# Performance work log

Hardware: AMD Instinct MI355X
Metric: run time of the kernel (lower is better)

## Reference

```python
import jax, jax.numpy as jnp
import numpy as np

DIM = 1024
HEADS = 16
HEAD_DIM = DIM // HEADS
K = 13              # kernel_size (odd)
NS = K // 2         # neighborhood radius
SCALE = HEAD_DIM ** -0.5


def setup_inputs() -> dict:
    key = jax.random.key(0)
    ks = jax.random.split(key, 5)
    B, L = 2, 4096
    x = jax.random.normal(ks[0], (B, L, DIM), jnp.float32)
    qkv_w = jax.random.normal(ks[1], (3 * DIM, DIM), jnp.float32) * 0.02
    qkv_b = jnp.zeros((3 * DIM,), jnp.float32)
    rpb = jax.random.normal(ks[2], (HEADS, 2 * K - 1), jnp.float32) * 0.02  # trunc_normal std=0.02
    proj_w = jax.random.normal(ks[3], (DIM, DIM), jnp.float32) * 0.02
    proj_b = jnp.zeros((DIM,), jnp.float32)
    return dict(x=x, qkv_w=qkv_w, qkv_b=qkv_b, rpb=rpb, proj_w=proj_w, proj_b=proj_b)


def reference(x, qkv_w, qkv_b, rpb, proj_w, proj_b):
    B, L, C = x.shape
    # qkv projection (torch Linear convention: y = x @ W^T + b)
    qkv = (x @ qkv_w.T + qkv_b).reshape(B, L, 3, HEADS, HEAD_DIM).transpose(2, 0, 3, 1, 4)
    q, k, v = qkv[0] * SCALE, qkv[1], qkv[2]  # each [B, H, L, D]

    i = jnp.arange(L)
    # NATTEN 1D window start (dilation=1): clamp window fully inside [0, L)
    ni = jnp.clip(i - NS, 0, L - K)                       # [L]
    # relative-position-bias start index per query (NATTEN get_pb_start)
    pi = NS + jnp.where(i < NS, NS - i, 0) + jnp.where(i + NS >= L, L - i - 1 - NS, 0)  # [L]
    j = jnp.arange(K)
    nbr = ni[:, None] + j[None, :]                        # [L, K] neighbor key indices
    bidx = pi[:, None] + j[None, :]                       # [L, K] rpb indices in [0, 2K-2]

    kg = k[:, :, nbr, :]                                  # [B, H, L, K, D]
    vg = v[:, :, nbr, :]                                  # [B, H, L, K, D]

    attn = jnp.einsum('bhld,bhlkd->bhlk', q, kg) + rpb[:, bidx][None]  # [B, H, L, K]
    attn = jax.nn.softmax(attn, axis=-1)
    out = jnp.einsum('bhlk,bhlkd->bhld', attn, vg)        # [B, H, L, D]
    out = out.transpose(0, 2, 1, 3).reshape(B, L, C)
    return out @ proj_w.T + proj_b
```

## Files before the change

### kernel.cpp

```cpp
#include <hip/hip_runtime.h>
#include <hip/hip_bf16.h>

#define DIMC 1024
#define HEADS 16
#define HEAD_DIM 64
#define KWIN 13
#define NSH 6
#define LSEQ 4096
#define BATCH 2
#define NROWS (BATCH*LSEQ)
#define QKV_N (3*DIMC)
#define SCALE_Q 0.125f

#define TBLK 256
#define WROWS 268

typedef __attribute__((ext_vector_type(4))) float f32x4;
typedef __attribute__((ext_vector_type(8))) short bf16x8;

__device__ __forceinline__ void gload_lds16(const void* g, void* l) {
  __builtin_amdgcn_global_load_lds(
      (const __attribute__((address_space(1))) void*)g,
      (__attribute__((address_space(3))) void*)l, 16, 0, 0);
}

__device__ __forceinline__ void cvt8(uint4 r, float* f) {
  unsigned u[4] = {r.x, r.y, r.z, r.w};
#pragma unroll
  for (int w = 0; w < 4; w++) {
    f[2*w]   = __uint_as_float(u[w] << 16);
    f[2*w+1] = __uint_as_float(u[w] & 0xffff0000u);
  }
}

__global__ __launch_bounds__(256) void cast3_kernel(const float* __restrict__ in0, __hip_bfloat16* __restrict__ out0, int n0,
                                                    const float* __restrict__ in1, __hip_bfloat16* __restrict__ out1, int n1,
                                                    const float* __restrict__ in2, __hip_bfloat16* __restrict__ out2, int n2) {
  int i = blockIdx.x * 256 + threadIdx.x;
  const float* in; __hip_bfloat16* out; int k;
  if (i < n0) { in = in0; out = out0; k = i; }
  else if (i < n0 + n1) { in = in1; out = out1; k = i - n0; }
  else if (i < n0 + n1 + n2) { in = in2; out = out2; k = i - n0 - n1; }
  else return;
  float4 v = ((const float4*)in)[k];
  union { short4 s; __hip_bfloat16 h[4]; } u;
  u.h[0] = __float2bfloat16(v.x);
  u.h[1] = __float2bfloat16(v.y);
  u.h[2] = __float2bfloat16(v.z);
  u.h[3] = __float2bfloat16(v.w);
  ((short4*)out)[k] = u.s;
}

template<int OUT_BF16>
__global__ __launch_bounds__(256) void gemm_bt(const __hip_bfloat16* __restrict__ A,
                                               const __hip_bfloat16* __restrict__ B,
                                               const float* __restrict__ bias,
                                               void* __restrict__ Cout,
                                               int M, int N, int K) {
  __shared__ __align__(16) __hip_bfloat16 smem[16384];
  __hip_bfloat16* As = smem;
  __hip_bfloat16* Bs = smem + 4096;

  const int tid  = threadIdx.x;
  const int lane = tid & 63;
  const int wave = tid >> 6;
  const int m0 = blockIdx.y * 128;
  const int n0 = blockIdx.x * 128;
  const int wr = wave >> 1;
  const int wc = wave & 1;

  f32x4 acc[4][4] = {};

  const int rA0  = wave * 32 + (lane >> 2);
  const int kcol = ((lane & 3) ^ ((lane >> 3) & 3)) * 8;
  const __hip_bfloat16* gA = A + (size_t)(m0 + rA0) * K + kcol;
  const __hip_bfloat16* gB = B + (size_t)(n0 + rA0) * K + kcol;
  __hip_bfloat16* lA0 = As + wave * 1024;
  __hip_bfloat16* lA1 = As + wave * 1024 + 512;
  __hip_bfloat16* lB0 = Bs + wave * 1024;
  __hip_bfloat16* lB1 = Bs + wave * 1024 + 512;

  const int fr  = lane & 15;
  const int fq  = lane >> 4;
  const int fk0 = ((fq ^ ((fr >> 1) & 3)) & 3) * 8;

  const size_t r16 = (size_t)16 * K;

  for (int k0 = 0; k0 < K; k0 += 64) {
    gload_lds16(gA,            lA0);
    gload_lds16(gA + r16,      lA1);
    gload_lds16(gB,            lB0);
    gload_lds16(gB + r16,      lB1);
    gload_lds16(gA + 32,       lA0 + 8192);
    gload_lds16(gA + r16 + 32, lA1 + 8192);
    gload_lds16(gB + 32,       lB0 + 8192);
    gload_lds16(gB + r16 + 32, lB1 + 8192);
    gA += 64;
    gB += 64;
    __syncthreads();

#pragma unroll
    for (int half = 0; half < 2; half++) {
      const int hb = half * 8192;
      bf16x8 af[4], bfr[4];
#pragma unroll
      for (int i = 0; i < 4; i++)
        af[i] = *(const bf16x8*)&As[hb + (wr * 64 + i * 16 + fr) * 32 + fk0];
#pragma unroll
      for (int i = 0; i < 4; i++)
        bfr[i] = *(const bf16x8*)&Bs[hb + (wc * 64 + i * 16 + fr) * 32 + fk0];

#pragma unroll
      for (int mi = 0; mi < 4; mi++)
#pragma unroll
        for (int ni = 0; ni < 4; ni++)
          acc[mi][ni] = __builtin_amdgcn_mfma_f32_16x16x32_bf16(af[mi], bfr[ni], acc[mi][ni], 0, 0, 0);
    }

    __syncthreads();
  }

#pragma unroll
  for (int ni = 0; ni < 4; ni++) {
    const int col = n0 + wc * 64 + ni * 16 + (lane & 15);
    const float bv = bias[col];
#pragma unroll
    for (int mi = 0; mi < 4; mi++) {
      const int row = m0 + wr * 64 + mi * 16 + ((lane >> 4) << 2);
#pragma unroll
      for (int i = 0; i < 4; i++) {
        const float v = acc[mi][ni][i] + bv;
        if (OUT_BF16)
          ((__hip_bfloat16*)Cout)[(size_t)(row + i) * N + col] = __float2bfloat16(v);
        else
          ((float*)Cout)[(size_t)(row + i) * N + col] = v;
      }
    }
  }
}

__global__ __launch_bounds__(256, 2) void natten(const __hip_bfloat16* __restrict__ qkv,
                                                 const float* __restrict__ rpb,
                                                 __hip_bfloat16* __restrict__ att) {
  __shared__ __align__(16) unsigned char smem[2 * WROWS * 128];

  const int tid = threadIdx.x;
  const int tb  = blockIdx.x;
  const int h   = blockIdx.y;
  const int b   = blockIdx.z;
  const int t0  = tb * TBLK;

  int r0 = t0 - NSH;
  if (r0 < 0) r0 = 0;
  if (r0 > LSEQ - WROWS) r0 = LSEQ - WROWS;

  const __hip_bfloat16* kg = qkv + ((size_t)b * LSEQ + r0) * QKV_N + DIMC + h * HEAD_DIM;
  const __hip_bfloat16* vg = kg + DIMC;
#pragma unroll 1
  for (int i = tid; i < WROWS * 8; i += 256) {
    const int row = i >> 3, c = i & 7;
    const uint4 kk = *(const uint4*)(kg + (size_t)row * QKV_N + c * 8);
    const uint4 vv = *(const uint4*)(vg + (size_t)row * QKV_N + c * 8);
    const int off = row * 128 + ((c * 16) ^ ((row & 7) << 4));
    *(uint4*)(smem + off) = kk;
    *(uint4*)(smem + WROWS * 128 + off) = vv;
  }
  __syncthreads();

  const int t = t0 + tid;
  int ni = t - NSH;
  ni = ni < 0 ? 0 : (ni > LSEQ - KWIN ? LSEQ - KWIN : ni);
  const int rbase = ni - r0;
  const int pi = NSH + (t < NSH ? NSH - t : 0) + (t + NSH >= LSEQ ? LSEQ - t - 1 - NSH : 0);
  const float* rp = rpb + h * (2 * KWIN - 1) + pi;

  const __hip_bfloat16* qg = qkv + ((size_t)b * LSEQ + t) * QKV_N + h * HEAD_DIM;
  float qf[64];
#pragma unroll
  for (int c = 0; c < 8; c++) {
    uint4 qq = *(const uint4*)(qg + c * 8);
    cvt8(qq, qf + c * 8);
  }

  float p[KWIN];
#pragma unroll
  for (int j = 0; j < KWIN; j++) {
    const int row = rbase + j;
    const int sw = (row & 7) << 4;
    float s = 0.f;
#pragma unroll
    for (int c = 0; c < 8; c++) {
      uint4 kk = *(const uint4*)(smem + row * 128 + ((c * 16) ^ sw));
      float kf[8];
      cvt8(kk, kf);
#pragma unroll
      for (int e = 0; e < 8; e++) s += qf[c * 8 + e] * kf[e];
    }
    p[j] = s * SCALE_Q + rp[j];
  }

  float m = p[0];
#pragma unroll
  for (int j = 1; j < KWIN; j++) m = fmaxf(m, p[j]);
  float sum = 0.f;
#pragma unroll
  for (int j = 0; j < KWIN; j++) { p[j] = __expf(p[j] - m); sum += p[j]; }
  const float inv = 1.f / sum;
#pragma unroll
  for (int j = 0; j < KWIN; j++) p[j] *= inv;

  __hip_bfloat16* og = att + ((size_t)b * LSEQ + t) * DIMC + h * HEAD_DIM;
#pragma unroll
  for (int c = 0; c < 8; c++) {
    float acc[8] = {0.f, 0.f, 0.f, 0.f, 0.f, 0.f, 0.f, 0.f};
#pragma unroll
    for (int j = 0; j < KWIN; j++) {
      const int row = rbase + j;
      uint4 vv = *(const uint4*)(smem + WROWS * 128 + row * 128 + ((c * 16) ^ ((row & 7) << 4)));
      float vf[8];
      cvt8(vv, vf);
#pragma unroll
      for (int e = 0; e < 8; e++) acc[e] += p[j] * vf[e];
    }
    union { ushort us[8]; uint4 v; } o;
#pragma unroll
    for (int e = 0; e < 8; e++) {
      __hip_bfloat16 hb = __float2bfloat16(acc[e]);
      o.us[e] = *(ushort*)&hb;
    }
    *(uint4*)(og + c * 8) = o.v;
  }
}

extern "C" void kernel_launch(void* const* d_in, const int* in_sizes, int n_in,
                              void* d_out, int out_size, void* d_ws, size_t ws_size,
                              hipStream_t stream) {
  const float* x      = (const float*)d_in[0];
  const float* qkv_w  = (const float*)d_in[1];
  const float* qkv_b  = (const float*)d_in[2];
  const float* rpb    = (const float*)d_in[3];
  const float* proj_w = (const float*)d_in[4];
  const float* proj_b = (const float*)d_in[5];
  float* out = (float*)d_out;

  char* ws = (char*)d_ws;
  __hip_bfloat16* xb    = (__hip_bfloat16*)(ws);
  __hip_bfloat16* wqkv  = (__hip_bfloat16*)(ws + 16777216);
  __hip_bfloat16* wproj = (__hip_bfloat16*)(ws + 23068672);
  __hip_bfloat16* qkv   = (__hip_bfloat16*)(ws + 25165824);
  __hip_bfloat16* att   = (__hip_bfloat16*)(ws + 75497472);

  const int n0 = NROWS * DIMC / 4;
  const int n1 = QKV_N * DIMC / 4;
  const int n2 = DIMC * DIMC / 4;
  cast3_kernel<<<(n0 + n1 + n2 + 255) / 256, 256, 0, stream>>>(
      x, xb, n0, qkv_w, wqkv, n1, proj_w, wproj, n2);

  gemm_bt<1><<<dim3(QKV_N / 128, NROWS / 128), 256, 0, stream>>>(
      xb, wqkv, qkv_b, (void*)qkv, NROWS, QKV_N, DIMC);

  natten<<<dim3(LSEQ / TBLK, HEADS, BATCH), 256, 0, stream>>>(qkv, rpb, att);

  gemm_bt<0><<<dim3(DIMC / 128, NROWS / 128), 256, 0, stream>>>(
      att, wproj, proj_b, (void*)out, NROWS, DIMC, DIMC);
}
```

Before: 138.4 us.

## Double-buffer GEMM LDS tiles to overlap global loads with MFMA

Restructures the GEMM main loop from a load-all-then-compute scheme with two syncs per 64-wide K step into a ping-pong double buffer over 32-wide K slices. The next slice's global-to-LDS loads are issued before computing on the current buffer, so there is one barrier per slice and memory latency is meant to hide behind the MFMAs. The shared memory size is unchanged, but the loop now runs twice as many iterations with less work in each, which may lower the instruction-level parallelism available between barriers.

```diff
diff --git a/kernel.cpp b/kernel.cpp
--- a/kernel.cpp
+++ b/kernel.cpp
@@ -51,6 +51,28 @@
   ((short4*)out)[k] = u.s;
 }
 
+
+#define STAGE4(s) do { \
+  __hip_bfloat16* dst_ = smem + (s) * 8192 + wave * 1024; \
+  gload_lds16(gA,       dst_); \
+  gload_lds16(gA + r16, dst_ + 512); \
+  gload_lds16(gB,       dst_ + 4096); \
+  gload_lds16(gB + r16, dst_ + 4096 + 512); \
+} while (0)
+
+#define COMPUTE16(s) do { \
+  const __hip_bfloat16* As_ = smem + (s) * 8192; \
+  const __hip_bfloat16* Bs_ = As_ + 4096; \
+  bf16x8 af[4], bfr[4]; \
+  _Pragma("unroll") for (int i = 0; i < 4; i++) \
+    af[i] = *(const bf16x8*)&As_[(wr * 64 + i * 16 + fr) * 32 + fk0]; \
+  _Pragma("unroll") for (int i = 0; i < 4; i++) \
+    bfr[i] = *(const bf16x8*)&Bs_[(wc * 64 + i * 16 + fr) * 32 + fk0]; \
+  _Pragma("unroll") for (int mi = 0; mi < 4; mi++) \
+  _Pragma("unroll") for (int ni = 0; ni < 4; ni++) \
+    acc[mi][ni] = __builtin_amdgcn_mfma_f32_16x16x32_bf16(af[mi], bfr[ni], acc[mi][ni], 0, 0, 0); \
+} while (0)
+
 template<int OUT_BF16>
 __global__ __launch_bounds__(256) void gemm_bt(const __hip_bfloat16* __restrict__ A,
                                                const __hip_bfloat16* __restrict__ B,
@@ -58,8 +80,6 @@
                                                void* __restrict__ Cout,
                                                int M, int N, int K) {
   __shared__ __align__(16) __hip_bfloat16 smem[16384];
-  __hip_bfloat16* As = smem;
-  __hip_bfloat16* Bs = smem + 4096;
 
   const int tid  = threadIdx.x;
   const int lane = tid & 63;
@@ -75,50 +95,28 @@
   const int kcol = ((lane & 3) ^ ((lane >> 3) & 3)) * 8;
   const __hip_bfloat16* gA = A + (size_t)(m0 + rA0) * K + kcol;
   const __hip_bfloat16* gB = B + (size_t)(n0 + rA0) * K + kcol;
-  __hip_bfloat16* lA0 = As + wave * 1024;
-  __hip_bfloat16* lA1 = As + wave * 1024 + 512;
-  __hip_bfloat16* lB0 = Bs + wave * 1024;
-  __hip_bfloat16* lB1 = Bs + wave * 1024 + 512;
+  const size_t r16 = (size_t)16 * K;
 
   const int fr  = lane & 15;
   const int fq  = lane >> 4;
   const int fk0 = ((fq ^ ((fr >> 1) & 3)) & 3) * 8;
 
-  const size_t r16 = (size_t)16 * K;
-
-  for (int k0 = 0; k0 < K; k0 += 64) {
-    gload_lds16(gA,            lA0);
-    gload_lds16(gA + r16,      lA1);
-    gload_lds16(gB,            lB0);
-    gload_lds16(gB + r16,      lB1);
-    gload_lds16(gA + 32,       lA0 + 8192);
-    gload_lds16(gA + r16 + 32, lA1 + 8192);
-    gload_lds16(gB + 32,       lB0 + 8192);
-    gload_lds16(gB + r16 + 32, lB1 + 8192);
-    gA += 64;
-    gB += 64;
+  const int NT = K >> 5;
+
+  STAGE4(0);
+  gA += 32; gB += 32;
+  __syncthreads();
+
+  int cur = 0;
+#pragma unroll 1
+  for (int t = 1; t < NT; t++) {
+    STAGE4(cur ^ 1);
+    gA += 32; gB += 32;
+    COMPUTE16(cur);
     __syncthreads();
-
-#pragma unroll
-    for (int half = 0; half < 2; half++) {
-      const int hb = half * 8192;
-      bf16x8 af[4], bfr[4];
-#pragma unroll
-      for (int i = 0; i < 4; i++)
-        af[i] = *(const bf16x8*)&As[hb + (wr * 64 + i * 16 + fr) * 32 + fk0];
-#pragma unroll
-      for (int i = 0; i < 4; i++)
-        bfr[i] = *(const bf16x8*)&Bs[hb + (wc * 64 + i * 16 + fr) * 32 + fk0];
-
-#pragma unroll
-      for (int mi = 0; mi < 4; mi++)
-#pragma unroll
-        for (int ni = 0; ni < 4; ni++)
-          acc[mi][ni] = __builtin_amdgcn_mfma_f32_16x16x32_bf16(af[mi], bfr[ni], acc[mi][ni], 0, 0, 0);
-    }
-
-    __syncthreads();
-  }
+    cur ^= 1;
+  }
+  COMPUTE16(cur);
 
 #pragma unroll
   for (int ni = 0; ni < 4; ni++) {
```

New measurement: 137.5 us. No clear change (-0.7%).
